# Kernel tuning notes

Hardware: AMD Instinct MI355X
Metric: run time of the kernel (lower is better)

## Reference

```python
import jax, jax.numpy as jnp
import numpy as np

N_HEADS = 16

def setup_inputs() -> dict:
    key = jax.random.key(0)
    kx, kk, kq, kv, ko = jax.random.split(key, 5)
    B, T, D = 8, 1024, 1024
    s = 1.0 / np.sqrt(D)
    return {
        'x':  jax.random.normal(kx, (B, T, D), dtype=jnp.float32),
        'Wk': jax.random.normal(kk, (D, D), dtype=jnp.float32) * s,
        'Wq': jax.random.normal(kq, (D, D), dtype=jnp.float32) * s,
        'Wv': jax.random.normal(kv, (D, D), dtype=jnp.float32) * s,
        'Wo': jax.random.normal(ko, (D, D), dtype=jnp.float32) * s,
    }

def reference(x, Wk, Wq, Wv, Wo):
    B, T, D = x.shape
    H = D // N_HEADS  # head dim
    # projections (nn.Linear with bias=False: y = x @ W^T)
    k = (x @ Wk.T).reshape(B, T, N_HEADS, H).transpose(0, 2, 1, 3)  # [B,n,T,H]
    q = (x @ Wq.T).reshape(B, T, N_HEADS, H).transpose(0, 2, 1, 3)
    v = (x @ Wv.T).reshape(B, T, N_HEADS, H).transpose(0, 2, 1, 3)
    scores = jnp.einsum('bnqh,bnkh->bnqk', q, k)                    # [B,n,T,T]
    causal = jnp.tril(jnp.ones((T, T), dtype=bool))
    # original: masked_fill(-inf) BEFORE scaling; -inf/sqrt(H) stays -inf
    scores = jnp.where(causal, scores, -jnp.inf) / jnp.sqrt(jnp.float32(H))
    att = jax.nn.softmax(scores, axis=-1)
    # dropout p=0.0 -> identity
    out = jnp.einsum('bnqk,bnkh->bnqh', att, v)                     # [B,n,T,H]
    out = out.transpose(0, 2, 1, 3).reshape(B, T, D)
    return out @ Wo.T
```

## Files before the change

kernel.cpp:

```cpp
#include <hip/hip_runtime.h>
#include <stdint.h>

typedef __bf16 bf16x8 __attribute__((ext_vector_type(8)));
typedef float f32x4 __attribute__((ext_vector_type(4)));
typedef unsigned short ushort_t;
typedef unsigned int uint_t;

__device__ inline ushort_t f2bf(float f) {
  uint_t u = __builtin_bit_cast(uint_t, f);
  u = (u + 0x7FFFu + ((u >> 16) & 1u)) >> 16;
  return (ushort_t)u;
}

__device__ inline void gll16(const void* g, void* l) {
  __builtin_amdgcn_global_load_lds(
      (__attribute__((address_space(1))) void*)(uintptr_t)g,
      (__attribute__((address_space(3))) void*)(uint32_t)(uintptr_t)l,
      16, 0, 0);
}

__global__ void cast_bf16(const float* __restrict__ in, ushort_t* __restrict__ out,
                          int n4, float scale) {
  int i = blockIdx.x * blockDim.x + threadIdx.x;
  int st = gridDim.x * blockDim.x;
  for (; i < n4; i += st) {
    float4 v = reinterpret_cast<const float4*>(in)[i];
    ushort4 o;
    o.x = f2bf(v.x * scale);
    o.y = f2bf(v.y * scale);
    o.z = f2bf(v.z * scale);
    o.w = f2bf(v.w * scale);
    reinterpret_cast<ushort4*>(out)[i] = o;
  }
}

__global__ void cast_w4(const float* __restrict__ w0, const float* __restrict__ w1,
                        const float* __restrict__ w2, const float* __restrict__ w3,
                        ushort_t* __restrict__ out, float s0) {
  const int i = blockIdx.x * 256 + threadIdx.x;
  const int which = i >> 18;
  const float* src = which == 0 ? w0 : which == 1 ? w1 : which == 2 ? w2 : w3;
  const float sc = which == 0 ? s0 : 1.0f;
  float4 v = reinterpret_cast<const float4*>(src)[i & 0x3FFFF];
  ushort4 o;
  o.x = f2bf(v.x * sc);
  o.y = f2bf(v.y * sc);
  o.z = f2bf(v.z * sc);
  o.w = f2bf(v.w * sc);
  reinterpret_cast<ushort4*>(out)[i] = o;
}

#define MFMA16(A_, B_, C_) __builtin_amdgcn_mfma_f32_16x16x32_bf16(A_, B_, C_, 0, 0, 0)

template <int MF, int NF, int NTN, int LDC, bool F32OUT>
__global__ __launch_bounds__(512, 2) void gemm8p(const ushort_t* __restrict__ A,
                                                 const ushort_t* __restrict__ B,
                                                 void* __restrict__ C) {
  constexpr int BM = MF * 32;
  constexpr int BN = NF * 64;
  constexpr int NA = BM / 64;
  constexpr int NB = BN / 64;
  constexpr int AU = BM * 64;
  constexpr int BUF = AU + BN * 64;
  constexpr int NWG = (8192 / BM) * NTN;
  __shared__ __attribute__((aligned(16))) ushort_t smem[2 * BUF];

  const int tid = threadIdx.x;
  const int lane = tid & 63;
  const int w = tid >> 6;
  const int wm = w >> 2, wn = w & 3;

  const int bid = blockIdx.x;
  const int swz = (bid & 7) * (NWG / 8) + (bid >> 3);
  const int m0 = (swz / NTN) * BM;
  const int n0 = (swz % NTN) * BN;

  const int scol = ((tid & 7) ^ ((tid >> 3) & 7)) * 8;
  const ushort_t* gA = A + (size_t)(m0 + (tid >> 3)) * 1024 + scol;
  const ushort_t* gB = B + (size_t)(n0 + (tid >> 3)) * 1024 + scol;

  const int lr = lane & 15;
  const int hi = lane >> 4;
  const int arow = (wm * MF * 16 + lr) * 64;
  const int brow = AU + (wn * NF * 16 + lr) * 64;
  const int cx0 = (hi * 8) ^ ((lane & 7) << 3);
  const int cx1 = cx0 ^ 32;

  f32x4 acc[MF][NF] = {};
  bf16x8 a[MF / 2][2], b[NF][2];

  auto stageA = [&](int wbu, int sk) __attribute__((always_inline)) {
#pragma unroll
    for (int i = 0; i < NA; ++i)
      gll16(gA + i * 65536 + sk, &smem[wbu + i * 4096 + (w << 9)]);
  };
  auto stageB = [&](int wbu, int sk) __attribute__((always_inline)) {
#pragma unroll
    for (int i = 0; i < NB; ++i)
      gll16(gB + i * 65536 + sk, &smem[wbu + AU + i * 4096 + (w << 9)]);
  };
  auto rdA = [&](int rbu, int mbase) __attribute__((always_inline)) {
#pragma unroll
    for (int m = 0; m < MF / 2; ++m) {
      const int base = rbu + arow + (mbase + m) * 1024;
      a[m][0] = *(const bf16x8*)&smem[base + cx0];
      a[m][1] = *(const bf16x8*)&smem[base + cx1];
    }
  };
  auto rdB = [&](int rbu) __attribute__((always_inline)) {
#pragma unroll
    for (int n = 0; n < NF; ++n) {
      const int base = rbu + brow + n * 1024;
      b[n][0] = *(const bf16x8*)&smem[base + cx0];
      b[n][1] = *(const bf16x8*)&smem[base + cx1];
    }
  };
  auto mm = [&](int mbase) __attribute__((always_inline)) {
#pragma unroll
    for (int m = 0; m < MF / 2; ++m)
#pragma unroll
      for (int n = 0; n < NF; ++n) {
        acc[mbase + m][n] = MFMA16(a[m][0], b[n][0], acc[mbase + m][n]);
        acc[mbase + m][n] = MFMA16(a[m][1], b[n][1], acc[mbase + m][n]);
      }
  };

  auto tile = [&](int rbu, int wbu, int sk, bool pf) __attribute__((always_inline)) {
    rdA(rbu, 0);
    rdB(rbu);
    if (pf) {
      stageA(wbu, sk);
      stageB(wbu, sk);
    }
    __builtin_amdgcn_s_barrier();
    asm volatile("s_waitcnt lgkmcnt(0)" ::: "memory");
    __builtin_amdgcn_s_setprio(1);
    mm(0);
    __builtin_amdgcn_s_setprio(0);
    __builtin_amdgcn_s_barrier();
    rdA(rbu, MF / 2);
    __builtin_amdgcn_s_barrier();
    asm volatile("s_waitcnt lgkmcnt(0)" ::: "memory");
    __builtin_amdgcn_s_setprio(1);
    mm(MF / 2);
    __builtin_amdgcn_s_setprio(0);
    if (pf) asm volatile("s_waitcnt vmcnt(0)" ::: "memory");
    __builtin_amdgcn_s_barrier();
  };

  stageA(0, 0);
  stageB(0, 0);
  asm volatile("s_waitcnt vmcnt(0)" ::: "memory");
  __builtin_amdgcn_s_barrier();
  int sk = 64;
  for (int it = 0; it < 7; ++it) {
    tile(0, BUF, sk, true);
    sk += 64;
    tile(BUF, 0, sk, true);
    sk += 64;
  }
  tile(0, BUF, sk, true);
  tile(BUF, 0, 0, false);

  const size_t erow = (size_t)(m0 + wm * MF * 16 + hi * 4);
  const int ecol = n0 + wn * NF * 16 + lr;
#pragma unroll
  for (int mf = 0; mf < MF; ++mf)
#pragma unroll
    for (int nf = 0; nf < NF; ++nf)
#pragma unroll
      for (int r = 0; r < 4; ++r) {
        const size_t idx = (erow + mf * 16 + r) * LDC + ecol + nf * 16;
        if constexpr (F32OUT)
          ((float*)C)[idx] = acc[mf][nf][r];
        else
          ((ushort_t*)C)[idx] = f2bf(acc[mf][nf][r]);
      }
}

__global__ __launch_bounds__(256, 2) void attn_fwd(const ushort_t* __restrict__ QKV,
                                                   ushort_t* __restrict__ ctx) {
  const int bid = blockIdx.x;
  const int h = bid & 15;
  const int b = (bid >> 4) & 7;
  const int p = bid >> 7;
  const int tid = threadIdx.x;
  const int lane = tid & 63;
  const int w = tid >> 6;
  const int lr = lane & 15;
  const int lg = lane >> 4;
  const int dk = lg << 3;

  __shared__ __attribute__((aligned(16))) ushort_t Ks[2][64 * 72];
  __shared__ __attribute__((aligned(16))) uint_t VtDw[2][64 * 36];
  __shared__ __attribute__((aligned(16))) ushort_t Pl[4][32 * 72];

  const int kkey = tid >> 2, kdg = tid & 3;
  const int vkp = tid & 31, vdg = tid >> 5;
  const ushort_t* kgbase =
      QKV + ((size_t)(b * 1024 + kkey)) * 3072 + 1024 + h * 64 + kdg * 16;
  const ushort_t* vgbase =
      QKV + ((size_t)(b * 1024 + 2 * vkp)) * 3072 + 2048 + h * 64 + vdg * 8;

  const float FMAX2 = 23.083120654223414f;

  for (int pi = 0; pi < 2; ++pi) {
    const int qt = pi ? (7 - p) : p;
    const int q0 = qt << 7;
    const int nt = (qt + 1) << 1;
    const int wrow0 = q0 + w * 32;

    bf16x8 qf[2][2];
#pragma unroll
    for (int i = 0; i < 2; ++i) {
      const ushort_t* qp =
          QKV + ((size_t)(b * 1024 + wrow0 + i * 16 + lr)) * 3072 + h * 64 + dk;
      qf[i][0] = *reinterpret_cast<const bf16x8*>(qp);
      qf[i][1] = *reinterpret_cast<const bf16x8*>(qp + 32);
    }

    f32x4 o[2][4] = {};
    float lsum[2] = {0.f, 0.f};

    uint4 rk0 = *reinterpret_cast<const uint4*>(kgbase);
    uint4 rk1 = *reinterpret_cast<const uint4*>(kgbase + 8);
    uint4 rv0 = *reinterpret_cast<const uint4*>(vgbase);
    uint4 rv1 = *reinterpret_cast<const uint4*>(vgbase + 3072);

    for (int t = 0; t < nt; ++t) {
      const int bsel = t & 1;
      asm volatile("s_waitcnt vmcnt(0)" ::: "memory");
      {
        uint_t* kd = reinterpret_cast<uint_t*>(&Ks[bsel][kkey * 72 + kdg * 16]);
        *reinterpret_cast<uint4*>(kd) = rk0;
        *reinterpret_cast<uint4*>(kd + 4) = rk1;
        const ushort_t* e0 = reinterpret_cast<const ushort_t*>(&rv0);
        const ushort_t* e1 = reinterpret_cast<const ushort_t*>(&rv1);
#pragma unroll
        for (int j = 0; j < 8; ++j)
          VtDw[bsel][(vdg * 8 + j) * 36 + vkp] = (uint_t)e0[j] | ((uint_t)e1[j] << 16);
      }
      if (t + 1 < nt) {
        const size_t off = (size_t)(t + 1) * 64 * 3072;
        rk0 = *reinterpret_cast<const uint4*>(kgbase + off);
        rk1 = *reinterpret_cast<const uint4*>(kgbase + off + 8);
        rv0 = *reinterpret_cast<const uint4*>(vgbase + off);
        rv1 = *reinterpret_cast<const uint4*>(vgbase + off + 3072);
      }
      asm volatile("s_waitcnt lgkmcnt(0)" ::: "memory");
      __builtin_amdgcn_s_barrier();

      const int kb = t << 6;
      if (kb > wrow0 + 31) continue;

      bf16x8 kf0[4], kf1[4];
#pragma unroll
      for (int f = 0; f < 4; ++f) {
        kf0[f] = *reinterpret_cast<const bf16x8*>(&Ks[bsel][(f * 16 + lr) * 72 + dk]);
        kf1[f] =
            *reinterpret_cast<const bf16x8*>(&Ks[bsel][(f * 16 + lr) * 72 + 32 + dk]);
      }
      f32x4 s[2][4];
#pragma unroll
      for (int i = 0; i < 2; ++i)
#pragma unroll
        for (int f = 0; f < 4; ++f) {
          f32x4 z = {0.f, 0.f, 0.f, 0.f};
          z = __builtin_amdgcn_mfma_f32_16x16x32_bf16(kf0[f], qf[i][0], z, 0, 0, 0);
          s[i][f] = __builtin_amdgcn_mfma_f32_16x16x32_bf16(kf1[f], qf[i][1], z, 0, 0, 0);
        }

      const bool needmask = (kb + 63 > wrow0);
#pragma unroll
      for (int i = 0; i < 2; ++i) {
        const int qr = wrow0 + i * 16 + lr;
#pragma unroll
        for (int f = 0; f < 4; ++f) {
          const int kbase = kb + f * 16 + (lg << 2);
          float p0 = __builtin_amdgcn_exp2f(s[i][f][0] - FMAX2);
          float p1 = __builtin_amdgcn_exp2f(s[i][f][1] - FMAX2);
          float p2 = __builtin_amdgcn_exp2f(s[i][f][2] - FMAX2);
          float p3 = __builtin_amdgcn_exp2f(s[i][f][3] - FMAX2);
          if (needmask) {
            p0 = (kbase + 0 <= qr) ? p0 : 0.f;
            p1 = (kbase + 1 <= qr) ? p1 : 0.f;
            p2 = (kbase + 2 <= qr) ? p2 : 0.f;
            p3 = (kbase + 3 <= qr) ? p3 : 0.f;
          }
          lsum[i] += (p0 + p1) + (p2 + p3);
          ushort4 pk = {f2bf(p0), f2bf(p1), f2bf(p2), f2bf(p3)};
          *reinterpret_cast<ushort4*>(
              &Pl[w][(i * 16 + lr) * 72 + f * 16 + (lg << 2)]) = pk;
        }
      }

      bf16x8 vb[2][4];
#pragma unroll
      for (int kblk = 0; kblk < 2; ++kblk)
#pragma unroll
        for (int fh = 0; fh < 4; ++fh)
          vb[kblk][fh] = *reinterpret_cast<const bf16x8*>(
              &VtDw[bsel][(fh * 16 + lr) * 36 + kblk * 16 + (lg << 2)]);
#pragma unroll
      for (int i = 0; i < 2; ++i)
#pragma unroll
        for (int kblk = 0; kblk < 2; ++kblk) {
          const bf16x8 pa = *reinterpret_cast<const bf16x8*>(
              &Pl[w][(i * 16 + lr) * 72 + kblk * 32 + dk]);
#pragma unroll
          for (int fh = 0; fh < 4; ++fh)
            o[i][fh] = __builtin_amdgcn_mfma_f32_16x16x32_bf16(pa, vb[kblk][fh],
                                                               o[i][fh], 0, 0, 0);
        }
    }

#pragma unroll
    for (int i = 0; i < 2; ++i) {
      float ls = lsum[i];
      ls += __shfl_xor(ls, 16);
      ls += __shfl_xor(ls, 32);
      const float linv = 1.0f / ls;
      const size_t crow = (size_t)(b * 1024 + wrow0 + i * 16 + (lg << 2));
#pragma unroll
      for (int r = 0; r < 4; ++r) {
        const float li = __shfl(linv, (lg << 2) + r);
#pragma unroll
        for (int fh = 0; fh < 4; ++fh)
          ctx[(crow + r) * 1024 + h * 64 + fh * 16 + lr] = f2bf(o[i][fh][r] * li);
      }
    }
  }
}

extern "C" void kernel_launch(void* const* d_in, const int* in_sizes, int n_in,
                              void* d_out, int out_size, void* d_ws, size_t ws_size,
                              hipStream_t stream) {
  const float* x = (const float*)d_in[0];
  const float* Wk = (const float*)d_in[1];
  const float* Wq = (const float*)d_in[2];
  const float* Wv = (const float*)d_in[3];
  const float* Wo = (const float*)d_in[4];

  char* ws = (char*)d_ws;
  ushort_t* xb = (ushort_t*)ws;
  ushort_t* Wc = (ushort_t*)(ws + (16u << 20));
  ushort_t* Wob = Wc + 3u * 1024 * 1024;
  ushort_t* QKV = (ushort_t*)(ws + (24u << 20));
  ushort_t* ctx = xb;

  cast_bf16<<<2048, 256, 0, stream>>>(x, xb, (8192 * 1024) / 4, 1.0f);
  cast_w4<<<4096, 256, 0, stream>>>(Wq, Wk, Wv, Wo, Wc, 0.125f * 1.4426950408889634f);

  gemm8p<8, 3, 16, 3072, false><<<512, 512, 0, stream>>>(xb, Wc, QKV);

  attn_fwd<<<512, 256, 0, stream>>>(QKV, ctx);

  gemm8p<4, 4, 4, 1024, true><<<256, 512, 0, stream>>>(ctx, Wob, (float*)d_out);
}
```

Measured before the change: 137.3 us.

## Split GEMM tile into two k-halves and stagger A/B prefetch with partial vmcnt waits

The per-tile compute now runs in two k-halves, each loading A and B fragments from LDS just before its MFMAs, which halves the fragment registers live at once. The A prefetch for the next tile is issued before the first half and the B prefetch after it, with partial vmcnt waits replacing full drains. The goal is to overlap global-to-LDS loads with MFMA work and spread out memory traffic. In exchange it adds barriers per tile and relies on delicate vmcnt counts, so a wrong count could race on the double buffer.

```diff
diff --git a/kernel.cpp b/kernel.cpp
--- a/kernel.cpp
+++ b/kernel.cpp
@@ -99,59 +99,71 @@
     for (int i = 0; i < NB; ++i)
       gll16(gB + i * 65536 + sk, &smem[wbu + AU + i * 4096 + (w << 9)]);
   };
-  auto rdA = [&](int rbu, int mbase) __attribute__((always_inline)) {
-#pragma unroll
-    for (int m = 0; m < MF / 2; ++m) {
-      const int base = rbu + arow + (mbase + m) * 1024;
-      a[m][0] = *(const bf16x8*)&smem[base + cx0];
-      a[m][1] = *(const bf16x8*)&smem[base + cx1];
-    }
-  };
-  auto rdB = [&](int rbu) __attribute__((always_inline)) {
-#pragma unroll
-    for (int n = 0; n < NF; ++n) {
-      const int base = rbu + brow + n * 1024;
-      b[n][0] = *(const bf16x8*)&smem[base + cx0];
-      b[n][1] = *(const bf16x8*)&smem[base + cx1];
-    }
-  };
-  auto mm = [&](int mbase) __attribute__((always_inline)) {
+  auto rdA = [&](int rbu, int mbase, int kk) __attribute__((always_inline)) {
+    const int cx = kk ? cx1 : cx0;
 #pragma unroll
     for (int m = 0; m < MF / 2; ++m)
-#pragma unroll
-      for (int n = 0; n < NF; ++n) {
-        acc[mbase + m][n] = MFMA16(a[m][0], b[n][0], acc[mbase + m][n]);
-        acc[mbase + m][n] = MFMA16(a[m][1], b[n][1], acc[mbase + m][n]);
-      }
+      a[m][kk] = *(const bf16x8*)&smem[rbu + arow + (mbase + m) * 1024 + cx];
+  };
+  auto rdB = [&](int rbu, int kk) __attribute__((always_inline)) {
+    const int cx = kk ? cx1 : cx0;
+#pragma unroll
+    for (int n = 0; n < NF; ++n)
+      b[n][kk] = *(const bf16x8*)&smem[rbu + brow + n * 1024 + cx];
+  };
+  auto mmk = [&](int mbase, int kk) __attribute__((always_inline)) {
+#pragma unroll
+    for (int m = 0; m < MF / 2; ++m)
+#pragma unroll
+      for (int n = 0; n < NF; ++n)
+        acc[mbase + m][n] = MFMA16(a[m][kk], b[n][kk], acc[mbase + m][n]);
   };
 
   auto tile = [&](int rbu, int wbu, int sk, bool pf) __attribute__((always_inline)) {
-    rdA(rbu, 0);
-    rdB(rbu);
     if (pf) {
       stageA(wbu, sk);
-      stageB(wbu, sk);
+      if constexpr (NA == 4)
+        asm volatile("s_waitcnt vmcnt(4)" ::: "memory");
+      else
+        asm volatile("s_waitcnt vmcnt(2)" ::: "memory");
+    } else {
+      asm volatile("s_waitcnt vmcnt(0)" ::: "memory");
     }
     __builtin_amdgcn_s_barrier();
+    rdA(rbu, 0, 0);
+    rdB(rbu, 0);
     asm volatile("s_waitcnt lgkmcnt(0)" ::: "memory");
     __builtin_amdgcn_s_setprio(1);
-    mm(0);
+    mmk(0, 0);
     __builtin_amdgcn_s_setprio(0);
     __builtin_amdgcn_s_barrier();
-    rdA(rbu, MF / 2);
+    rdA(rbu, MF / 2, 0);
     __builtin_amdgcn_s_barrier();
     asm volatile("s_waitcnt lgkmcnt(0)" ::: "memory");
     __builtin_amdgcn_s_setprio(1);
-    mm(MF / 2);
+    mmk(MF / 2, 0);
     __builtin_amdgcn_s_setprio(0);
-    if (pf) asm volatile("s_waitcnt vmcnt(0)" ::: "memory");
+    __builtin_amdgcn_s_barrier();
+    rdA(rbu, 0, 1);
+    rdB(rbu, 1);
+    if (pf) stageB(wbu, sk);
+    __builtin_amdgcn_s_barrier();
+    asm volatile("s_waitcnt lgkmcnt(0)" ::: "memory");
+    __builtin_amdgcn_s_setprio(1);
+    mmk(0, 1);
+    __builtin_amdgcn_s_setprio(0);
+    __builtin_amdgcn_s_barrier();
+    rdA(rbu, MF / 2, 1);
+    __builtin_amdgcn_s_barrier();
+    asm volatile("s_waitcnt lgkmcnt(0)" ::: "memory");
+    __builtin_amdgcn_s_setprio(1);
+    mmk(MF / 2, 1);
+    __builtin_amdgcn_s_setprio(0);
     __builtin_amdgcn_s_barrier();
   };
 
   stageA(0, 0);
   stageB(0, 0);
-  asm volatile("s_waitcnt vmcnt(0)" ::: "memory");
-  __builtin_amdgcn_s_barrier();
   int sk = 64;
   for (int it = 0; it < 7; ++it) {
     tile(0, BUF, sk, true);
```

Result: no change. 137.9 us (+0.4%).

## Interleave staged global loads with MFMA quarters using fine-grained vmcnt waits

Applied to the files above, without the earlier changes.

Splits each K-tile of the bf16 GEMM into four MFMA quarters (A halves × B column groups) and spreads the global-to-LDS prefetches for the next tile across those quarters. Partial vmcnt waits replace the full drain at tile end, so loads overlap compute and issue pressure is spread out. The counting of outstanding loads is delicate: a wrong vmcnt value or the extra barriers could cause races or stalls.

```diff
diff --git a/kernel.cpp b/kernel.cpp
--- a/kernel.cpp
+++ b/kernel.cpp
@@ -51,6 +51,8 @@
 }
 
 #define MFMA16(A_, B_, C_) __builtin_amdgcn_mfma_f32_16x16x32_bf16(A_, B_, C_, 0, 0, 0)
+#define SBAR __builtin_amdgcn_s_barrier
+#define LGKM0 asm volatile("s_waitcnt lgkmcnt(0)" ::: "memory")
 
 template <int MF, int NF, int NTN, int LDC, bool F32OUT>
 __global__ __launch_bounds__(512, 2) void gemm8p(const ushort_t* __restrict__ A,
@@ -60,6 +62,8 @@
   constexpr int BN = NF * 64;
   constexpr int NA = BM / 64;
   constexpr int NB = BN / 64;
+  constexpr int NB0 = 2;
+  constexpr int NG0 = 2;
   constexpr int AU = BM * 64;
   constexpr int BUF = AU + BN * 64;
   constexpr int NWG = (8192 / BM) * NTN;
@@ -87,16 +91,33 @@
   const int cx1 = cx0 ^ 32;
 
   f32x4 acc[MF][NF] = {};
-  bf16x8 a[MF / 2][2], b[NF][2];
-
-  auto stageA = [&](int wbu, int sk) __attribute__((always_inline)) {
-#pragma unroll
-    for (int i = 0; i < NA; ++i)
-      gll16(gA + i * 65536 + sk, &smem[wbu + i * 4096 + (w << 9)]);
-  };
-  auto stageB = [&](int wbu, int sk) __attribute__((always_inline)) {
-#pragma unroll
-    for (int i = 0; i < NB; ++i)
+  bf16x8 a[MF / 2][2];
+  bf16x8 b[NF][2];
+
+  auto stage_a_even = [&](int wbu, int sk) __attribute__((always_inline)) {
+    if constexpr (MF == 8) {
+      gll16(gA + 0 * 65536 + sk, &smem[wbu + 0 * 4096 + (w << 9)]);
+      gll16(gA + 2 * 65536 + sk, &smem[wbu + 2 * 4096 + (w << 9)]);
+    } else {
+#pragma unroll
+      for (int i = 0; i < NA; ++i)
+        gll16(gA + i * 65536 + sk, &smem[wbu + i * 4096 + (w << 9)]);
+    }
+  };
+  auto stage_a_odd = [&](int wbu, int sk) __attribute__((always_inline)) {
+    if constexpr (MF == 8) {
+      gll16(gA + 1 * 65536 + sk, &smem[wbu + 1 * 4096 + (w << 9)]);
+      gll16(gA + 3 * 65536 + sk, &smem[wbu + 3 * 4096 + (w << 9)]);
+    }
+  };
+  auto stage_b0 = [&](int wbu, int sk) __attribute__((always_inline)) {
+#pragma unroll
+    for (int i = 0; i < NB0; ++i)
+      gll16(gB + i * 65536 + sk, &smem[wbu + AU + i * 4096 + (w << 9)]);
+  };
+  auto stage_b1 = [&](int wbu, int sk) __attribute__((always_inline)) {
+#pragma unroll
+    for (int i = NB0; i < NB; ++i)
       gll16(gB + i * 65536 + sk, &smem[wbu + AU + i * 4096 + (w << 9)]);
   };
   auto rdA = [&](int rbu, int mbase) __attribute__((always_inline)) {
@@ -107,51 +128,82 @@
       a[m][1] = *(const bf16x8*)&smem[base + cx1];
     }
   };
-  auto rdB = [&](int rbu) __attribute__((always_inline)) {
+  auto rdBg = [&](int rbu, int ng0, int ng1) __attribute__((always_inline)) {
 #pragma unroll
     for (int n = 0; n < NF; ++n) {
+      if (n < ng0 || n >= ng1) continue;
       const int base = rbu + brow + n * 1024;
       b[n][0] = *(const bf16x8*)&smem[base + cx0];
       b[n][1] = *(const bf16x8*)&smem[base + cx1];
     }
   };
-  auto mm = [&](int mbase) __attribute__((always_inline)) {
+  auto mmg = [&](int mbase, int ng0, int ng1) __attribute__((always_inline)) {
 #pragma unroll
     for (int m = 0; m < MF / 2; ++m)
 #pragma unroll
       for (int n = 0; n < NF; ++n) {
+        if (n < ng0 || n >= ng1) continue;
         acc[mbase + m][n] = MFMA16(a[m][0], b[n][0], acc[mbase + m][n]);
         acc[mbase + m][n] = MFMA16(a[m][1], b[n][1], acc[mbase + m][n]);
       }
   };
 
   auto tile = [&](int rbu, int wbu, int sk, bool pf) __attribute__((always_inline)) {
+    if (pf) {
+      stage_a_even(wbu, sk);
+      if constexpr (MF == 8)
+        asm volatile("s_waitcnt vmcnt(4)" ::: "memory");
+      else
+        asm volatile("s_waitcnt vmcnt(2)" ::: "memory");
+    } else {
+      if constexpr (MF == 8)
+        asm volatile("s_waitcnt vmcnt(2)" ::: "memory");
+      else
+        asm volatile("s_waitcnt vmcnt(0)" ::: "memory");
+    }
+    SBAR();
     rdA(rbu, 0);
-    rdB(rbu);
+    rdBg(rbu, 0, NG0);
+    LGKM0;
+    __builtin_amdgcn_s_setprio(1);
+    mmg(0, 0, NG0);
+    __builtin_amdgcn_s_setprio(0);
+    SBAR();
+    rdBg(rbu, NG0, NF);
+    if (pf) stage_b0(wbu, sk);
+    SBAR();
+    LGKM0;
+    __builtin_amdgcn_s_setprio(1);
+    mmg(0, NG0, NF);
+    __builtin_amdgcn_s_setprio(0);
+    SBAR();
     if (pf) {
-      stageA(wbu, sk);
-      stageB(wbu, sk);
-    }
-    __builtin_amdgcn_s_barrier();
-    asm volatile("s_waitcnt lgkmcnt(0)" ::: "memory");
+      stage_b1(wbu, sk);
+      if constexpr (MF == 8)
+        asm volatile("s_waitcnt vmcnt(5)" ::: "memory");
+    } else {
+      if constexpr (MF == 8)
+        asm volatile("s_waitcnt vmcnt(0)" ::: "memory");
+    }
+    SBAR();
+    rdA(rbu, MF / 2);
+    LGKM0;
     __builtin_amdgcn_s_setprio(1);
-    mm(0);
+    mmg(MF / 2, NG0, NF);
     __builtin_amdgcn_s_setprio(0);
-    __builtin_amdgcn_s_barrier();
-    rdA(rbu, MF / 2);
-    __builtin_amdgcn_s_barrier();
-    asm volatile("s_waitcnt lgkmcnt(0)" ::: "memory");
+    SBAR();
+    if (pf) stage_a_odd(wbu, sk);
+    SBAR();
     __builtin_amdgcn_s_setprio(1);
-    mm(MF / 2);
+    mmg(MF / 2, 0, NG0);
     __builtin_amdgcn_s_setprio(0);
-    if (pf) asm volatile("s_waitcnt vmcnt(0)" ::: "memory");
-    __builtin_amdgcn_s_barrier();
-  };
-
-  stageA(0, 0);
-  stageB(0, 0);
-  asm volatile("s_waitcnt vmcnt(0)" ::: "memory");
-  __builtin_amdgcn_s_barrier();
+    SBAR();
+  };
+
+  stage_a_even(0, 0);
+  stage_b0(0, 0);
+  stage_b1(0, 0);
+  stage_a_odd(0, 0);
   int sk = 64;
   for (int it = 0; it < 7; ++it) {
     tile(0, BUF, sk, true);
```

Measured after the change: 135.8 us. About the same (-1.1%).
